# Performance work log

Hardware: AMD Instinct MI355X
Metric: run time of the kernel (lower is better)

The kernel has to match this reference:

```python
import jax, jax.numpy as jnp
import numpy as np

L, D, HQ, HKV, HD, P, V, B, S = 4, 2048, 16, 4, 128, 8192, 32000, 2, 1024
THETA, EPS = 500000.0, 1e-5
RATIO = HQ // HKV  # GQA q-to-kv ratio = 4


def rmsnorm(x, w):
    # torch: w * (x * rsqrt(mean(x^2, -1) + eps)) computed in fp32
    x32 = x.astype(jnp.float32)
    n = x32 * jax.lax.rsqrt(jnp.mean(x32 * x32, axis=-1, keepdims=True) + EPS)
    return w * n.astype(x.dtype)


def make_rope(seq_len):
    inv = 1.0 / (THETA ** (jnp.arange(0, HD, 2, dtype=jnp.float32) / HD))  # [HD/2]
    ang = jnp.arange(seq_len, dtype=jnp.float32)[:, None] * inv[None, :]   # [S, HD/2]
    return jnp.cos(ang)[None, :, None, :], jnp.sin(ang)[None, :, None, :]  # [1,S,1,HD/2]


def rope(t, cos, sin):
    # torch code: complex = t[..., :HD/2] + i*t[..., HD/2:], multiply by e^{i*ang},
    # then view_as_real + flatten -> INTERLEAVED (r0,i0,r1,i1,...) output layout.
    h = HD // 2
    r, im = t[..., :h], t[..., h:]
    orr = r * cos - im * sin
    oim = r * sin + im * cos
    return jnp.stack([orr, oim], axis=-1).reshape(t.shape)


def attention(x, wqkv, wo, cos, sin):
    b, s, _ = x.shape
    qkv = x @ wqkv                               # [b,s,D+2*HKV*HD]
    q = qkv[..., :D].reshape(b, s, HQ, HD)
    k = qkv[..., D:D + HKV * HD].reshape(b, s, HKV, HD)
    v = qkv[..., D + HKV * HD:].reshape(b, s, HKV, HD)
    q = rope(q, cos, sin)
    k = rope(k, cos, sin)
    # GQA: repeat_interleave kv heads to match q heads (offset=0 prefill; cache is identity)
    k = jnp.repeat(k, RATIO, axis=2)
    v = jnp.repeat(v, RATIO, axis=2)
    scale = 1.0 / np.sqrt(HD)
    scores = jnp.einsum('bqhd,bkhd->bhqk', q, k) * scale
    causal = jnp.tril(jnp.ones((s, s), dtype=bool))
    scores = jnp.where(causal[None, None], scores, jnp.finfo(scores.dtype).min)
    probs = jax.nn.softmax(scores, axis=-1)
    out = jnp.einsum('bhqk,bkhd->bqhd', probs, v).reshape(b, s, D)
    return out @ wo


def swiglu(x, wgu, wd):
    gu = x @ wgu                                  # [b,s,2P]
    gate, up = gu[..., :P], gu[..., P:]
    return (jax.nn.silu(gate) * up) @ wd


def setup_inputs() -> dict:
    key = jax.random.key(0)
    ks = jax.random.split(key, 8)
    sc = 0.02
    return {
        'tokens': jax.random.randint(ks[0], (B, S), 0, V),
        'emb': jax.random.normal(ks[1], (V, D), jnp.float32) * sc,
        'w_qkv': jax.random.normal(ks[2], (L, D, D + 2 * HKV * HD), jnp.float32) * sc,
        'w_o': jax.random.normal(ks[3], (L, D, D), jnp.float32) * sc,
        'w_gate_up': jax.random.normal(ks[4], (L, D, 2 * P), jnp.float32) * sc,
        'w_down': jax.random.normal(ks[5], (L, P, D), jnp.float32) * sc,
        'ln_attn': jnp.ones((L, D), jnp.float32),
        'ln_ffn': jnp.ones((L, D), jnp.float32),
        'ln_f': jnp.ones((D,), jnp.float32),
        'w_lm': jax.random.normal(ks[6], (D, V), jnp.float32) * sc,
    }


def reference(tokens, emb, w_qkv, w_o, w_gate_up, w_down, ln_attn, ln_ffn, ln_f, w_lm):
    cos, sin = make_rope(S)
    x = emb[tokens]                               # [B,S,D]
    for l in range(L):
        x = x + attention(rmsnorm(x, ln_attn[l]), w_qkv[l], w_o[l], cos, sin)
        x = x + swiglu(rmsnorm(x, ln_ffn[l]), w_gate_up[l], w_down[l])
    return rmsnorm(x, ln_f) @ w_lm                # logits [B,S,V]
```

## Files before the change

kernel.cpp:

```cpp
#include <hip/hip_runtime.h>
#include <hip/hip_bf16.h>
#include <math.h>

#define S_LEN 1024
#define DIM   2048
#define NHQ   16
#define NHKV  4
#define HDIM  128
#define PDIM  8192
#define VOCAB 32000
#define NLAYER 4
#define NROWS (2 * S_LEN)

typedef __attribute__((ext_vector_type(4))) float f32x4;
typedef __attribute__((ext_vector_type(8))) short bf16x8;

__device__ __forceinline__ void gload_lds16(const void* g, void* l) {
  __builtin_amdgcn_global_load_lds(
      (const __attribute__((address_space(1))) unsigned int*)g,
      (__attribute__((address_space(3))) unsigned int*)l, 16, 0, 0);
}

#define FENCE() asm volatile("" ::: "memory")

__global__ __launch_bounds__(256) void k_embed(const int* __restrict__ tokens,
    const float* __restrict__ emb, float* __restrict__ x) {
  int row = blockIdx.x;
  int tok = tokens[row];
  const f32x4* src = (const f32x4*)(emb + (size_t)tok * DIM);
  f32x4* dst = (f32x4*)(x + (size_t)row * DIM);
  for (int i = threadIdx.x; i < DIM / 4; i += 256) dst[i] = src[i];
}

__global__ __launch_bounds__(256) void k_rmsnorm(const float* __restrict__ x,
    const float* __restrict__ w, __hip_bfloat16* __restrict__ out) {
  int row = blockIdx.x;
  const float* xr = x + (size_t)row * DIM;
  float ss = 0.f;
  for (int i = threadIdx.x; i < DIM; i += 256) { float v = xr[i]; ss += v * v; }
  for (int off = 32; off; off >>= 1) ss += __shfl_xor(ss, off);
  __shared__ float wsum[4];
  if ((threadIdx.x & 63) == 0) wsum[threadIdx.x >> 6] = ss;
  __syncthreads();
  float tot = wsum[0] + wsum[1] + wsum[2] + wsum[3];
  float r = rsqrtf(tot / (float)DIM + 1e-5f);
  __hip_bfloat16* orow = out + (size_t)row * DIM;
  for (int i = threadIdx.x; i < DIM; i += 256)
    orow[i] = __float2bfloat16(w[i] * (xr[i] * r));
}

__global__ __launch_bounds__(256) void k_wt(const float* __restrict__ W,
    __hip_bfloat16* __restrict__ WT, int K, int N) {
  __shared__ __hip_bfloat16 t[64][72];
  int k0 = blockIdx.y * 64, n0 = blockIdx.x * 64;
  int r = threadIdx.x >> 4;
  int c4 = (threadIdx.x & 15) * 4;
#pragma unroll
  for (int i = 0; i < 4; ++i) {
    int k = r + i * 16;
    f32x4 v = *(const f32x4*)(W + (size_t)(k0 + k) * N + n0 + c4);
#pragma unroll
    for (int j = 0; j < 4; ++j) t[c4 + j][k] = __float2bfloat16(v[j]);
  }
  __syncthreads();
  int n = threadIdx.x >> 2, kc = (threadIdx.x & 3) * 16;
  bf16x8* dst = (bf16x8*)(WT + (size_t)(n0 + n) * K + k0 + kc);
  dst[0] = *(const bf16x8*)&t[n][kc];
  dst[1] = *(const bf16x8*)&t[n][kc + 8];
}

template<int EPI>
__global__ __launch_bounds__(512) void k_gemm256(
    const __hip_bfloat16* __restrict__ A, const __hip_bfloat16* __restrict__ BT,
    void* __restrict__ Cv, int M, int N, int K) {
  __shared__ __hip_bfloat16 AsH[4][128][64];
  __shared__ __hip_bfloat16 BsH[4][128][64];
  const int NH = K >> 5;
  int tid = threadIdx.x;
  int bid = blockIdx.x;
  int mt = bid & 7, nt = bid >> 3;
  int bm = mt << 8, bn = nt << 8;
  int wave = tid >> 6, lane = tid & 63;
  int wm = wave >> 2, wn = wave & 3;
  int g = lane >> 4, c = lane & 15;
  f32x4 acc[8][4] = {};

  int pre  = (lane & 7) ^ (lane >> 3);
  int rOff = (lane >> 3) * 2 + (pre >> 2);
  int cOff = (pre & 3) * 8;

  auto stageA = [&](int S, int h) {
#pragma unroll
    for (int rd = 0; rd < 2; ++rd) {
      int seg = rd * 8 + wave;
      gload_lds16(A + (size_t)(bm + seg * 16 + rOff) * K + h * 32 + cOff,
                  &AsH[S][seg * 8 + (lane >> 3)][(lane & 7) * 8]);
    }
  };
  auto stageB = [&](int S, int h) {
#pragma unroll
    for (int rd = 0; rd < 2; ++rd) {
      int seg = rd * 8 + wave;
      gload_lds16(BT + (size_t)(bn + seg * 16 + rOff) * K + h * 32 + cOff,
                  &BsH[S][seg * 8 + (lane >> 3)][(lane & 7) * 8]);
    }
  };

  stageA(0, 0); stageB(0, 0);
  stageA(1, 1); stageB(1, 1);
  stageA(2, 2);
  asm volatile("s_waitcnt vmcnt(6)" ::: "memory");
  __builtin_amdgcn_s_barrier();
  FENCE();

  int lineA = wm * 64 + (c >> 1);
  int lineB = wn * 32 + (c >> 1);
  int slotE = ((((c & 1) << 2) | g) ^ (c >> 1)) * 8;

  for (int H = 0; H < NH; ++H) {
    int S = H & 3;
    bf16x8 af[8], bv[4];
#pragma unroll
    for (int mi = 0; mi < 8; ++mi)
      af[mi] = *(const bf16x8*)&AsH[S][lineA + mi * 8][slotE];
#pragma unroll
    for (int ni = 0; ni < 4; ++ni)
      bv[ni] = *(const bf16x8*)&BsH[S][lineB + ni * 8][slotE];
    FENCE();
    if (H + 2 < NH) stageB((H + 2) & 3, H + 2);
    if (H + 3 < NH) stageA((H + 3) & 3, H + 3);
    if (H + 4 <= NH)      { asm volatile("s_waitcnt vmcnt(6)" ::: "memory"); }
    else if (H + 3 == NH) { asm volatile("s_waitcnt vmcnt(4)" ::: "memory"); }
    else if (H + 2 == NH) { asm volatile("s_waitcnt vmcnt(0)" ::: "memory"); }
    __builtin_amdgcn_s_barrier();
    asm volatile("s_waitcnt lgkmcnt(0)" ::: "memory");
    __builtin_amdgcn_sched_barrier(0);
    __builtin_amdgcn_s_setprio(1);
#pragma unroll
    for (int mi = 0; mi < 8; ++mi)
#pragma unroll
      for (int ni = 0; ni < 4; ++ni)
        acc[mi][ni] = __builtin_amdgcn_mfma_f32_16x16x32_bf16(af[mi], bv[ni], acc[mi][ni], 0, 0, 0);
    __builtin_amdgcn_s_setprio(0);
    FENCE();
    __builtin_amdgcn_s_barrier();
    FENCE();
  }

  float* Cf = (float*)Cv;
  __hip_bfloat16* Cb = (__hip_bfloat16*)Cv;
  int row0 = bm + wm * 128, col0 = bn + wn * 64;
#pragma unroll
  for (int mi = 0; mi < 8; ++mi)
#pragma unroll
    for (int ni = 0; ni < 4; ++ni)
#pragma unroll
      for (int r = 0; r < 4; ++r) {
        int row = row0 + mi * 16 + g * 4 + r;
        int col = col0 + ni * 16 + c;
        size_t idx = (size_t)row * N + col;
        if (EPI == 0) Cf[idx] = acc[mi][ni][r];
        else if (EPI == 1) Cf[idx] += acc[mi][ni][r];
        else Cb[idx] = __float2bfloat16(acc[mi][ni][r]);
      }
}

template<int EPI>
__global__ __launch_bounds__(256) void k_gemm_bt(
    const __hip_bfloat16* __restrict__ A, const __hip_bfloat16* __restrict__ BT,
    void* __restrict__ Cv, int M, int N, int K) {
  __shared__ __hip_bfloat16 As[2][128][64];
  __shared__ __hip_bfloat16 Bs[2][128][64];
  int nm = M >> 7;
  int bid = blockIdx.x;
  int mt, nt;
  if (nm == 16) {
    int xcd = bid & 7;
    int seq = bid >> 3;
    mt = (xcd << 1) | (seq & 1);
    nt = seq >> 1;
  } else {
    mt = bid % nm;
    nt = bid / nm;
  }
  int bm = mt << 7, bn = nt << 7;
  int tid  = threadIdx.x;
  int wave = tid >> 6, lane = tid & 63;
  int wr = (wave >> 1) * 64, wc = (wave & 1) * 64;
  int g = lane >> 4, c = lane & 15;
  f32x4 acc[4][4] = {};

  auto stage = [&](int buf, int k0) {
#pragma unroll
    for (int i = 0; i < 4; ++i) {
      int ci = i * 256 + tid;
      int row = ci >> 3, pc = ci & 7;
      int jl = pc ^ (row & 7);
      gload_lds16(A + (size_t)(bm + row) * K + k0 + jl * 8, &As[buf][row][pc * 8]);
      gload_lds16(BT + (size_t)(bn + row) * K + k0 + jl * 8, &Bs[buf][row][pc * 8]);
    }
  };

  int ntiles = K >> 6;
  stage(0, 0);
  if (ntiles > 1) stage(1, 64);

  for (int t = 0; t < ntiles; ++t) {
    int cur = t & 1;
    if (t + 1 < ntiles) asm volatile("s_waitcnt vmcnt(8)" ::: "memory");
    else                asm volatile("s_waitcnt vmcnt(0)" ::: "memory");
    __builtin_amdgcn_s_barrier();
    FENCE();
    __builtin_amdgcn_sched_barrier(0);
#pragma unroll
    for (int kk = 0; kk < 2; ++kk) {
      bf16x8 af[4], bv[4];
#pragma unroll
      for (int mi = 0; mi < 4; ++mi) {
        int row = wr + mi * 16 + c;
        int ch = (kk * 4 + g) ^ (row & 7);
        af[mi] = *(const bf16x8*)&As[cur][row][ch * 8];
      }
#pragma unroll
      for (int ni = 0; ni < 4; ++ni) {
        int row = wc + ni * 16 + c;
        int ch = (kk * 4 + g) ^ (row & 7);
        bv[ni] = *(const bf16x8*)&Bs[cur][row][ch * 8];
      }
      __builtin_amdgcn_s_setprio(1);
#pragma unroll
      for (int mi = 0; mi < 4; ++mi)
#pragma unroll
        for (int ni = 0; ni < 4; ++ni)
          acc[mi][ni] = __builtin_amdgcn_mfma_f32_16x16x32_bf16(af[mi], bv[ni], acc[mi][ni], 0, 0, 0);
      __builtin_amdgcn_s_setprio(0);
    }
    FENCE();
    __builtin_amdgcn_s_barrier();
    FENCE();
    if (t + 2 < ntiles) stage(cur, (t + 2) << 6);
  }

  float* Cf = (float*)Cv;
  __hip_bfloat16* Cb = (__hip_bfloat16*)Cv;
#pragma unroll
  for (int mi = 0; mi < 4; ++mi)
#pragma unroll
    for (int ni = 0; ni < 4; ++ni)
#pragma unroll
      for (int r = 0; r < 4; ++r) {
        int row = bm + wr + mi * 16 + g * 4 + r;
        int col = bn + wc + ni * 16 + c;
        size_t idx = (size_t)row * N + col;
        if (EPI == 0) Cf[idx] = acc[mi][ni][r];
        else if (EPI == 1) Cf[idx] += acc[mi][ni][r];
        else Cb[idx] = __float2bfloat16(acc[mi][ni][r]);
      }
}

template<int EPI>
__global__ __launch_bounds__(256) void k_gemm(
    const __hip_bfloat16* __restrict__ A, const float* __restrict__ Bw,
    void* __restrict__ Cv, int M, int N, int K) {
  __shared__ __hip_bfloat16 As[128][32];
  __shared__ __hip_bfloat16 Bs[128][40];
  int tid  = threadIdx.x;
  int bm = blockIdx.y * 128, bn = blockIdx.x * 128;
  int wave = tid >> 6, lane = tid & 63;
  int wr = (wave >> 1) * 64, wc = (wave & 1) * 64;
  int lrow = lane & 15, lk = (lane >> 4) * 8;
  f32x4 acc[4][4] = {};
  for (int k0 = 0; k0 < K; k0 += 32) {
#pragma unroll
    for (int i = 0; i < 2; ++i) {
      int L = i * 256 + tid;
      int row = L >> 2, koff = (L & 3) * 8;
      gload_lds16(A + (size_t)(bm + row) * K + k0 + koff, &As[row][koff]);
    }
#pragma unroll
    for (int i = 0; i < 4; ++i) {
      int L = i * 256 + tid;
      int kk = L >> 5;
      int c4 = (L & 31) * 4;
      f32x4 v = *(const f32x4*)(Bw + (size_t)(k0 + kk) * N + bn + c4);
#pragma unroll
      for (int j = 0; j < 4; ++j) Bs[c4 + j][kk] = __float2bfloat16(v[j]);
    }
    __syncthreads();
    bf16x8 af[4], bfr[4];
#pragma unroll
    for (int mi = 0; mi < 4; ++mi)
      af[mi] = *(const bf16x8*)(&As[wr + mi * 16 + lrow][lk]);
#pragma unroll
    for (int ni = 0; ni < 4; ++ni)
      bfr[ni] = *(const bf16x8*)(&Bs[wc + ni * 16 + lrow][lk]);
#pragma unroll
    for (int mi = 0; mi < 4; ++mi)
#pragma unroll
      for (int ni = 0; ni < 4; ++ni)
        acc[mi][ni] = __builtin_amdgcn_mfma_f32_16x16x32_bf16(af[mi], bfr[ni], acc[mi][ni], 0, 0, 0);
    __syncthreads();
  }
  float* Cf = (float*)Cv;
  __hip_bfloat16* Cb = (__hip_bfloat16*)Cv;
#pragma unroll
  for (int mi = 0; mi < 4; ++mi)
#pragma unroll
    for (int ni = 0; ni < 4; ++ni)
#pragma unroll
      for (int r = 0; r < 4; ++r) {
        int row = bm + wr + mi * 16 + ((lane >> 4) * 4 + r);
        int col = bn + wc + ni * 16 + (lane & 15);
        size_t idx = (size_t)row * N + col;
        if (EPI == 0) Cf[idx] = acc[mi][ni][r];
        else if (EPI == 1) Cf[idx] += acc[mi][ni][r];
        else Cb[idx] = __float2bfloat16(acc[mi][ni][r]);
      }
}

__global__ __launch_bounds__(256) void k_rope(const float* __restrict__ qkv,
    __hip_bfloat16* __restrict__ qr, __hip_bfloat16* __restrict__ kr,
    __hip_bfloat16* __restrict__ vt) {
  int rowid = blockIdx.x;
  int b = rowid >> 10, s = rowid & (S_LEN - 1);
  const float* src = qkv + (size_t)rowid * 3072;
  const float kInvLog = 0.20503692777f;
  const float scale = 0.08838834764831845f;
  __shared__ float cs[64], sn[64];
  if (threadIdx.x < 64) {
    float inv = expf(-(float)threadIdx.x * kInvLog);
    float a = (float)s * inv;
    sincosf(a, &sn[threadIdx.x], &cs[threadIdx.x]);
  }
  __syncthreads();
  for (int it = threadIdx.x; it < NHQ * 64; it += 256) {
    int h = it >> 6, i = it & 63;
    float re = src[h * HDIM + i], im = src[h * HDIM + 64 + i];
    size_t dst = ((size_t)(b * NHQ + h) * S_LEN + s) * HDIM;
    qr[dst + 2 * i]     = __float2bfloat16((re * cs[i] - im * sn[i]) * scale);
    qr[dst + 2 * i + 1] = __float2bfloat16((re * sn[i] + im * cs[i]) * scale);
  }
  for (int it = threadIdx.x; it < NHKV * 64; it += 256) {
    int h = it >> 6, i = it & 63;
    float re = src[DIM + h * HDIM + i], im = src[DIM + h * HDIM + 64 + i];
    size_t dst = ((size_t)(b * NHKV + h) * S_LEN + s) * HDIM;
    kr[dst + 2 * i]     = __float2bfloat16(re * cs[i] - im * sn[i]);
    kr[dst + 2 * i + 1] = __float2bfloat16(re * sn[i] + im * cs[i]);
  }
  for (int it = threadIdx.x; it < NHKV * HDIM; it += 256) {
    int h = it >> 7, d = it & 127;
    vt[(((size_t)b * NHKV + h) * HDIM + d) * S_LEN + s] =
        __float2bfloat16(src[DIM + NHKV * HDIM + it]);
  }
}

__global__ __launch_bounds__(256) void k_attn_mfma(
    const __hip_bfloat16* __restrict__ Q,
    const __hip_bfloat16* __restrict__ Kc,
    const __hip_bfloat16* __restrict__ VT,
    __hip_bfloat16* __restrict__ O) {
  __shared__ __hip_bfloat16 plds[4][16][40];
  int wave = threadIdx.x >> 6, lane = threadIdx.x & 63;
  int gw = blockIdx.x * 4 + wave;
  int qt = gw & 63;
  int bh = gw >> 6;
  int b = bh >> 4, h = bh & 15;
  int hk = h >> 2;
  int q0 = qt * 16;
  int g = lane >> 4, c = lane & 15;
  const __hip_bfloat16* Qb = Q + ((size_t)bh * S_LEN + q0) * HDIM;
  const __hip_bfloat16* Kb = Kc + (size_t)(b * NHKV + hk) * S_LEN * HDIM;
  const __hip_bfloat16* Vb = VT + (size_t)(b * NHKV + hk) * S_LEN * HDIM;

  bf16x8 qf[4];
#pragma unroll
  for (int cn = 0; cn < 4; ++cn)
    qf[cn] = *(const bf16x8*)(Qb + (size_t)c * HDIM + cn * 32 + g * 8);

  f32x4 po[8] = {};
  float m[4], l[4];
#pragma unroll
  for (int r = 0; r < 4; ++r) { m[r] = -1e30f; l[r] = 0.f; }

  int kvend = q0 + 16;
  for (int kv0 = 0; kv0 < kvend; kv0 += 32) {
    f32x4 s0 = {}, s1 = {};
#pragma unroll
    for (int cn = 0; cn < 4; ++cn) {
      bf16x8 k0f = *(const bf16x8*)(Kb + (size_t)(kv0 + c) * HDIM + cn * 32 + g * 8);
      bf16x8 k1f = *(const bf16x8*)(Kb + (size_t)(kv0 + 16 + c) * HDIM + cn * 32 + g * 8);
      s0 = __builtin_amdgcn_mfma_f32_16x16x32_bf16(qf[cn], k0f, s0, 0, 0, 0);
      s1 = __builtin_amdgcn_mfma_f32_16x16x32_bf16(qf[cn], k1f, s1, 0, 0, 0);
    }
    if (kv0 + 31 > q0) {
#pragma unroll
      for (int r = 0; r < 4; ++r) {
        int qrow = q0 + g * 4 + r;
        if (kv0 + c > qrow)      s0[r] = -1e30f;
        if (kv0 + 16 + c > qrow) s1[r] = -1e30f;
      }
    }
    float rm[4];
#pragma unroll
    for (int r = 0; r < 4; ++r) rm[r] = fmaxf(s0[r], s1[r]);
#pragma unroll
    for (int off = 1; off < 16; off <<= 1)
#pragma unroll
      for (int r = 0; r < 4; ++r) rm[r] = fmaxf(rm[r], __shfl_xor(rm[r], off));
    float p0[4], p1[4], rs[4];
#pragma unroll
    for (int r = 0; r < 4; ++r) {
      float mn = fmaxf(m[r], rm[r]);
      float corr = __expf(m[r] - mn);
      m[r] = mn;
      p0[r] = __expf(s0[r] - mn);
      p1[r] = __expf(s1[r] - mn);
      rs[r] = p0[r] + p1[r];
      l[r] *= corr;
#pragma unroll
      for (int t = 0; t < 8; ++t) po[t][r] *= corr;
    }
#pragma unroll
    for (int off = 1; off < 16; off <<= 1)
#pragma unroll
      for (int r = 0; r < 4; ++r) rs[r] += __shfl_xor(rs[r], off);
#pragma unroll
    for (int r = 0; r < 4; ++r) l[r] += rs[r];
#pragma unroll
    for (int r = 0; r < 4; ++r) {
      plds[wave][g * 4 + r][c]      = __float2bfloat16(p0[r]);
      plds[wave][g * 4 + r][16 + c] = __float2bfloat16(p1[r]);
    }
    bf16x8 pf = *(const bf16x8*)&plds[wave][c][g * 8];
#pragma unroll
    for (int t = 0; t < 8; ++t) {
      bf16x8 vf = *(const bf16x8*)(Vb + (size_t)(t * 16 + c) * S_LEN + kv0 + g * 8);
      po[t] = __builtin_amdgcn_mfma_f32_16x16x32_bf16(pf, vf, po[t], 0, 0, 0);
    }
  }
  float inv[4];
#pragma unroll
  for (int r = 0; r < 4; ++r) inv[r] = 1.f / l[r];
  __hip_bfloat16* ob = O + ((size_t)(b * S_LEN) + q0) * DIM + h * HDIM;
#pragma unroll
  for (int t = 0; t < 8; ++t)
#pragma unroll
    for (int r = 0; r < 4; ++r)
      ob[(size_t)(g * 4 + r) * DIM + t * 16 + c] = __float2bfloat16(po[t][r] * inv[r]);
}

__global__ __launch_bounds__(256) void k_swiglu(const __hip_bfloat16* __restrict__ gu,
    __hip_bfloat16* __restrict__ h) {
  size_t i = (size_t)blockIdx.x * 256 + threadIdx.x;
  size_t row = i >> 10, c8 = (i & 1023) * 8;
  const __hip_bfloat16* grow = gu + row * (2 * PDIM);
  bf16x8 gv = *(const bf16x8*)(grow + c8);
  bf16x8 uv = *(const bf16x8*)(grow + PDIM + c8);
  const __hip_bfloat16* gp = (const __hip_bfloat16*)&gv;
  const __hip_bfloat16* up = (const __hip_bfloat16*)&uv;
  __hip_bfloat16 ov[8];
#pragma unroll
  for (int j = 0; j < 8; ++j) {
    float g = __bfloat162float(gp[j]);
    float u = __bfloat162float(up[j]);
    float s = g / (1.f + __expf(-g));
    ov[j] = __float2bfloat16(s * u);
  }
  *(bf16x8*)(h + row * PDIM + c8) = *(const bf16x8*)ov;
}

extern "C" void kernel_launch(void* const* d_in, const int* in_sizes, int n_in,
                              void* d_out, int out_size, void* d_ws, size_t ws_size,
                              hipStream_t stream) {
  const int*   tokens    = (const int*)d_in[0];
  const float* emb       = (const float*)d_in[1];
  const float* w_qkv     = (const float*)d_in[2];
  const float* w_o       = (const float*)d_in[3];
  const float* w_gate_up = (const float*)d_in[4];
  const float* w_down    = (const float*)d_in[5];
  const float* ln_attn   = (const float*)d_in[6];
  const float* ln_ffn    = (const float*)d_in[7];
  const float* ln_f      = (const float*)d_in[8];
  const float* w_lm      = (const float*)d_in[9];
  float* out = (float*)d_out;

  char* ws = (char*)d_ws;
  float* x = (float*)ws;                    ws += (size_t)NROWS * DIM * 4;
  __hip_bfloat16* xn = (__hip_bfloat16*)ws; ws += (size_t)NROWS * DIM * 2;
  float* qkv = (float*)ws;                  ws += (size_t)NROWS * 3072 * 4;
  __hip_bfloat16* qr = (__hip_bfloat16*)ws; ws += (size_t)2 * NHQ * S_LEN * HDIM * 2;
  __hip_bfloat16* kr = (__hip_bfloat16*)ws; ws += (size_t)2 * NHKV * S_LEN * HDIM * 2;
  __hip_bfloat16* vt = (__hip_bfloat16*)ws; ws += (size_t)2 * NHKV * S_LEN * HDIM * 2;
  __hip_bfloat16* ao = (__hip_bfloat16*)ws; ws += (size_t)NROWS * DIM * 2;
  __hip_bfloat16* gu = (__hip_bfloat16*)ws; ws += (size_t)NROWS * 2 * PDIM * 2;
  __hip_bfloat16* hb = (__hip_bfloat16*)ws; ws += (size_t)NROWS * PDIM * 2;
  __hip_bfloat16* wbuf = (__hip_bfloat16*)ws;
  size_t need = (size_t)(ws - (char*)d_ws) + (size_t)VOCAB * DIM * 2;
  bool bf16w = ws_size >= need;

  k_embed<<<NROWS, 256, 0, stream>>>(tokens, emb, x);

  for (int l = 0; l < NLAYER; ++l) {
    k_rmsnorm<<<NROWS, 256, 0, stream>>>(x, ln_attn + (size_t)l * DIM, xn);
    if (bf16w) {
      k_wt<<<dim3(3072 / 64, DIM / 64), 256, 0, stream>>>(
          w_qkv + (size_t)l * DIM * 3072, wbuf, DIM, 3072);
      k_gemm_bt<0><<<(NROWS / 128) * (3072 / 128), 256, 0, stream>>>(
          xn, wbuf, qkv, NROWS, 3072, DIM);
    } else {
      k_gemm<0><<<dim3(3072 / 128, NROWS / 128), 256, 0, stream>>>(
          xn, w_qkv + (size_t)l * DIM * 3072, qkv, NROWS, 3072, DIM);
    }
    k_rope<<<NROWS, 256, 0, stream>>>(qkv, qr, kr, vt);
    k_attn_mfma<<<(2 * NHQ * (S_LEN / 16)) / 4, 256, 0, stream>>>(qr, kr, vt, ao);
    if (bf16w) {
      k_wt<<<dim3(DIM / 64, DIM / 64), 256, 0, stream>>>(
          w_o + (size_t)l * DIM * DIM, wbuf, DIM, DIM);
      k_gemm_bt<1><<<(NROWS / 128) * (DIM / 128), 256, 0, stream>>>(
          ao, wbuf, x, NROWS, DIM, DIM);
    } else {
      k_gemm<1><<<dim3(DIM / 128, NROWS / 128), 256, 0, stream>>>(
          ao, w_o + (size_t)l * DIM * DIM, x, NROWS, DIM, DIM);
    }
    k_rmsnorm<<<NROWS, 256, 0, stream>>>(x, ln_ffn + (size_t)l * DIM, xn);
    if (bf16w) {
      k_wt<<<dim3(2 * PDIM / 64, DIM / 64), 256, 0, stream>>>(
          w_gate_up + (size_t)l * DIM * 2 * PDIM, wbuf, DIM, 2 * PDIM);
      k_gemm256<2><<<8 * (2 * PDIM / 256), 512, 0, stream>>>(
          xn, wbuf, gu, NROWS, 2 * PDIM, DIM);
    } else {
      k_gemm<2><<<dim3(2 * PDIM / 128, NROWS / 128), 256, 0, stream>>>(
          xn, w_gate_up + (size_t)l * DIM * 2 * PDIM, gu, NROWS, 2 * PDIM, DIM);
    }
    k_swiglu<<<(NROWS * PDIM / 8) / 256, 256, 0, stream>>>(gu, hb);
    if (bf16w) {
      k_wt<<<dim3(DIM / 64, PDIM / 64), 256, 0, stream>>>(
          w_down + (size_t)l * PDIM * DIM, wbuf, PDIM, DIM);
      k_gemm_bt<1><<<(NROWS / 128) * (DIM / 128), 256, 0, stream>>>(
          hb, wbuf, x, NROWS, DIM, PDIM);
    } else {
      k_gemm<1><<<dim3(DIM / 128, NROWS / 128), 256, 0, stream>>>(
          hb, w_down + (size_t)l * PDIM * DIM, x, NROWS, DIM, PDIM);
    }
  }

  k_rmsnorm<<<NROWS, 256, 0, stream>>>(x, ln_f, xn);
  if (bf16w) {
    k_wt<<<dim3(VOCAB / 64, DIM / 64), 256, 0, stream>>>(w_lm, wbuf, DIM, VOCAB);
    k_gemm256<0><<<8 * (VOCAB / 256), 512, 0, stream>>>(
        xn, wbuf, out, NROWS, VOCAB, DIM);
  } else {
    k_gemm<0><<<dim3(VOCAB / 128, NROWS / 128), 256, 0, stream>>>(
        xn, w_lm, out, NROWS, VOCAB, DIM);
  }
}
```

Baseline: 2.697 ms.

## Restructure GEMM main loop into half-tile phases with finer prefetch interleaving

```diff
diff --git a/kernel.cpp b/kernel.cpp
--- a/kernel.cpp
+++ b/kernel.cpp
@@ -75,7 +75,7 @@
     void* __restrict__ Cv, int M, int N, int K) {
   __shared__ __hip_bfloat16 AsH[4][128][64];
   __shared__ __hip_bfloat16 BsH[4][128][64];
-  const int NH = K >> 5;
+  const int NT = K >> 6;
   int tid = threadIdx.x;
   int bid = blockIdx.x;
   int mt = bid & 7, nt = bid >> 3;
@@ -89,7 +89,8 @@
   int rOff = (lane >> 3) * 2 + (pre >> 2);
   int cOff = (pre & 3) * 8;
 
-  auto stageA = [&](int S, int h) {
+  auto stageA = [&](int h) {
+    int S = h & 3;
 #pragma unroll
     for (int rd = 0; rd < 2; ++rd) {
       int seg = rd * 8 + wave;
@@ -97,7 +98,8 @@
                   &AsH[S][seg * 8 + (lane >> 3)][(lane & 7) * 8]);
     }
   };
-  auto stageB = [&](int S, int h) {
+  auto stageB = [&](int h) {
+    int S = h & 3;
 #pragma unroll
     for (int rd = 0; rd < 2; ++rd) {
       int seg = rd * 8 + wave;
@@ -106,10 +108,10 @@
     }
   };
 
-  stageA(0, 0); stageB(0, 0);
-  stageA(1, 1); stageB(1, 1);
-  stageA(2, 2);
-  asm volatile("s_waitcnt vmcnt(6)" ::: "memory");
+  stageA(0); stageB(0); stageA(1); stageB(1);
+  if (NT > 1) { stageB(2); stageA(2); stageB(3); }
+  if (NT > 1) asm volatile("s_waitcnt vmcnt(10)" ::: "memory");
+  else        asm volatile("s_waitcnt vmcnt(0)"  ::: "memory");
   __builtin_amdgcn_s_barrier();
   FENCE();
 
@@ -117,31 +119,89 @@
   int lineB = wn * 32 + (c >> 1);
   int slotE = ((((c & 1) << 2) | g) ^ (c >> 1)) * 8;
 
-  for (int H = 0; H < NH; ++H) {
-    int S = H & 3;
-    bf16x8 af[8], bv[4];
-#pragma unroll
-    for (int mi = 0; mi < 8; ++mi)
-      af[mi] = *(const bf16x8*)&AsH[S][lineA + mi * 8][slotE];
+  bf16x8 af[4], bv[4];
+  for (int t = 0; t < NT; ++t) {
+    int S0 = (2 * t) & 3, S1 = (2 * t + 1) & 3;
+    bool steady = (t + 2 < NT);
+#pragma unroll
+    for (int mi = 0; mi < 4; ++mi)
+      af[mi] = *(const bf16x8*)&AsH[S0][lineA + mi * 8][slotE];
 #pragma unroll
     for (int ni = 0; ni < 4; ++ni)
-      bv[ni] = *(const bf16x8*)&BsH[S][lineB + ni * 8][slotE];
-    FENCE();
-    if (H + 2 < NH) stageB((H + 2) & 3, H + 2);
-    if (H + 3 < NH) stageA((H + 3) & 3, H + 3);
-    if (H + 4 <= NH)      { asm volatile("s_waitcnt vmcnt(6)" ::: "memory"); }
-    else if (H + 3 == NH) { asm volatile("s_waitcnt vmcnt(4)" ::: "memory"); }
-    else if (H + 2 == NH) { asm volatile("s_waitcnt vmcnt(0)" ::: "memory"); }
+      bv[ni] = *(const bf16x8*)&BsH[S0][lineB + ni * 8][slotE];
+    FENCE();
+    if (t + 1 < NT) stageA(2 * t + 3);
     __builtin_amdgcn_s_barrier();
     asm volatile("s_waitcnt lgkmcnt(0)" ::: "memory");
     __builtin_amdgcn_sched_barrier(0);
     __builtin_amdgcn_s_setprio(1);
 #pragma unroll
-    for (int mi = 0; mi < 8; ++mi)
+    for (int mi = 0; mi < 4; ++mi)
 #pragma unroll
       for (int ni = 0; ni < 4; ++ni)
         acc[mi][ni] = __builtin_amdgcn_mfma_f32_16x16x32_bf16(af[mi], bv[ni], acc[mi][ni], 0, 0, 0);
     __builtin_amdgcn_s_setprio(0);
+    FENCE();
+    __builtin_amdgcn_s_barrier();
+    FENCE();
+#pragma unroll
+    for (int mi = 0; mi < 4; ++mi)
+      af[mi] = *(const bf16x8*)&AsH[S0][lineA + 32 + mi * 8][slotE];
+    FENCE();
+    if (steady) stageB(2 * t + 4);
+    __builtin_amdgcn_s_barrier();
+    asm volatile("s_waitcnt lgkmcnt(0)" ::: "memory");
+    __builtin_amdgcn_sched_barrier(0);
+    __builtin_amdgcn_s_setprio(1);
+#pragma unroll
+    for (int mi = 0; mi < 4; ++mi)
+#pragma unroll
+      for (int ni = 0; ni < 4; ++ni)
+        acc[4 + mi][ni] = __builtin_amdgcn_mfma_f32_16x16x32_bf16(af[mi], bv[ni], acc[4 + mi][ni], 0, 0, 0);
+    __builtin_amdgcn_s_setprio(0);
+    if (steady) asm volatile("s_waitcnt vmcnt(10)" ::: "memory");
+    else        asm volatile("s_waitcnt vmcnt(0)"  ::: "memory");
+    FENCE();
+    __builtin_amdgcn_s_barrier();
+    FENCE();
+#pragma unroll
+    for (int mi = 0; mi < 4; ++mi)
+      af[mi] = *(const bf16x8*)&AsH[S1][lineA + mi * 8][slotE];
+#pragma unroll
+    for (int ni = 0; ni < 4; ++ni)
+      bv[ni] = *(const bf16x8*)&BsH[S1][lineB + ni * 8][slotE];
+    FENCE();
+    if (steady) stageA(2 * t + 4);
+    __builtin_amdgcn_s_barrier();
+    asm volatile("s_waitcnt lgkmcnt(0)" ::: "memory");
+    __builtin_amdgcn_sched_barrier(0);
+    __builtin_amdgcn_s_setprio(1);
+#pragma unroll
+    for (int mi = 0; mi < 4; ++mi)
+#pragma unroll
+      for (int ni = 0; ni < 4; ++ni)
+        acc[mi][ni] = __builtin_amdgcn_mfma_f32_16x16x32_bf16(af[mi], bv[ni], acc[mi][ni], 0, 0, 0);
+    __builtin_amdgcn_s_setprio(0);
+    FENCE();
+    __builtin_amdgcn_s_barrier();
+    FENCE();
+#pragma unroll
+    for (int mi = 0; mi < 4; ++mi)
+      af[mi] = *(const bf16x8*)&AsH[S1][lineA + 32 + mi * 8][slotE];
+    FENCE();
+    if (steady) stageB(2 * t + 5);
+    __builtin_amdgcn_s_barrier();
+    asm volatile("s_waitcnt lgkmcnt(0)" ::: "memory");
+    __builtin_amdgcn_sched_barrier(0);
+    __builtin_amdgcn_s_setprio(1);
+#pragma unroll
+    for (int mi = 0; mi < 4; ++mi)
+#pragma unroll
+      for (int ni = 0; ni < 4; ++ni)
+        acc[4 + mi][ni] = __builtin_amdgcn_mfma_f32_16x16x32_bf16(af[mi], bv[ni], acc[4 + mi][ni], 0, 0, 0);
+    __builtin_amdgcn_s_setprio(0);
+    if (steady) asm volatile("s_waitcnt vmcnt(10)" ::: "memory");
+    else        asm volatile("s_waitcnt vmcnt(0)"  ::: "memory");
     FENCE();
     __builtin_amdgcn_s_barrier();
     FENCE();
```

Result: no change. 2.734 ms (+1.4%).
